# Kernel tuning notes

Measured on AMD Instinct MI355X. Metric: run time of the kernel, lower is better.

Reference implementation:

```python
import jax, jax.numpy as jnp
import numpy as np

D_IN = 1024
D_OUT = 1024
SEQ = 2048
BATCH = 4


def setup_inputs() -> dict:
    key = jax.random.key(0)
    kx, kq, kk, kv = jax.random.split(key, 4)
    x = jax.random.normal(kx, (BATCH, SEQ, D_IN), dtype=jnp.float32)
    s = 1.0 / np.sqrt(D_IN)
    Wq = jax.random.uniform(kq, (D_IN, D_OUT), dtype=jnp.float32, minval=-s, maxval=s)
    Wk = jax.random.uniform(kk, (D_IN, D_OUT), dtype=jnp.float32, minval=-s, maxval=s)
    Wv = jax.random.uniform(kv, (D_IN, D_OUT), dtype=jnp.float32, minval=-s, maxval=s)
    return {"x": x, "Wq": Wq, "Wk": Wk, "Wv": Wv}


def reference(x, Wq, Wk, Wv):
    d_k = Wq.shape[1]
    q = jnp.einsum('bsd,de->bse', x, Wq)
    k = jnp.einsum('bsd,de->bse', x, Wk)
    v = jnp.einsum('bsd,de->bse', x, Wv)
    # [B, S, S] raw scores
    scores = jnp.einsum('bqe,bke->bqk', q, k)
    S = scores.shape[-1]
    causal = jnp.triu(jnp.ones((S, S), dtype=bool), k=1)  # True above diagonal
    scores = jnp.where(causal, -jnp.inf, scores)
    attn = jax.nn.softmax(scores * (d_k ** -0.5), axis=-1)
    # dropout p=0.0 -> identity
    return jnp.einsum('bqk,bke->bqe', attn, v)
```

## Files before the change

### kernel.cpp

```cpp
#include <hip/hip_runtime.h>
#include <hip/hip_bf16.h>

typedef unsigned short u16;
typedef __bf16 bfx8 __attribute__((ext_vector_type(8)));
typedef float fx4 __attribute__((ext_vector_type(4)));

#define SEQ 2048
#define DIM 1024
#define NBATCH 4
#define SCALE 0.03125f
#define NEL ((size_t)NBATCH * SEQ * DIM)

__device__ inline u16 f2bf(float f) {
    __bf16 h = (__bf16)f;
    return __builtin_bit_cast(unsigned short, h);
}

#define GLL(gp, lp) __builtin_amdgcn_global_load_lds( \
    (const __attribute__((address_space(1))) unsigned int*)(gp), \
    (__attribute__((address_space(3))) unsigned int*)(lp), 16, 0, 0)

__global__ __launch_bounds__(256) void prep(
    const float* __restrict__ X,
    const float* __restrict__ Wq, const float* __restrict__ Wk,
    const float* __restrict__ Wv,
    u16* __restrict__ XB, u16* __restrict__ WB, u16* __restrict__ WTv,
    float* __restrict__ Lrow)
{
    __shared__ u16 t[32][33];
    int bid = blockIdx.x;
    int tid = threadIdx.x;
    if (bid < 8192) {
        size_t i = (size_t)bid * 256 + tid;
        float4 v = ((const float4*)X)[i];
        uint2 pk;
        pk.x = (unsigned)f2bf(v.x) | ((unsigned)f2bf(v.y) << 16);
        pk.y = (unsigned)f2bf(v.z) | ((unsigned)f2bf(v.w) << 16);
        ((uint2*)XB)[i] = pk;
    } else if (bid < 10240) {
        int b2 = bid - 8192;
        const float* W = (b2 < 1024) ? Wq : Wk;
        u16* out = WB + (size_t)(b2 >> 10) * 1024 * 1024;
        size_t i = (size_t)(b2 & 1023) * 256 + tid;
        float4 v = ((const float4*)W)[i];
        uint2 pk;
        pk.x = (unsigned)f2bf(v.x) | ((unsigned)f2bf(v.y) << 16);
        pk.y = (unsigned)f2bf(v.z) | ((unsigned)f2bf(v.w) << 16);
        ((uint2*)out)[i] = pk;
    } else if (bid < 11264) {
        int t2 = bid - 10240;
        int n0 = (t2 & 31) * 32, k0 = (t2 >> 5) * 32;
        int tx = tid & 31, ty = tid >> 5;
        #pragma unroll
        for (int i = 0; i < 32; i += 8)
            t[ty + i][tx] = f2bf(Wv[(size_t)(k0 + ty + i) * 1024 + n0 + tx]);
        __syncthreads();
        #pragma unroll
        for (int i = 0; i < 32; i += 8)
            WTv[(size_t)(n0 + ty + i) * 1024 + k0 + tx] = t[tx][ty + i];
    } else {
        int i = (bid - 11264) * 256 + tid;
        Lrow[i] = 0.0f;
    }
}

__global__ __launch_bounds__(256) void gemm_m(
    const u16* __restrict__ WBk, const u16* __restrict__ WBq, u16* __restrict__ MT)
{
    int m0 = blockIdx.y * 128, n0 = blockIdx.x * 128;
    __shared__ __align__(16) u16 As[128 * 32];
    __shared__ __align__(16) u16 Bs[128 * 32];
    int tid = threadIdx.x, lane = tid & 63, w = tid >> 6;
    int wm = w >> 1, wn = w & 1, lo = lane & 15, qd = lane >> 4;
    fx4 acc[4][4] = {};

    int c0 = tid, c1 = tid + 256;
    const u16* a0 = WBk + (size_t)(m0 + (c0 >> 2)) * 1024 + (((c0 & 3) ^ ((c0 >> 2) & 3)) * 8);
    const u16* a1 = WBk + (size_t)(m0 + (c1 >> 2)) * 1024 + (((c1 & 3) ^ ((c1 >> 2) & 3)) * 8);
    const u16* b0 = WBq + (size_t)(n0 + (c0 >> 2)) * 1024 + (((c0 & 3) ^ ((c0 >> 2) & 3)) * 8);
    const u16* b1 = WBq + (size_t)(n0 + (c1 >> 2)) * 1024 + (((c1 & 3) ^ ((c1 >> 2) & 3)) * 8);

    int sw = (qd ^ (lo & 3)) * 8;
    for (int k0 = 0; k0 < 1024; k0 += 32) {
        GLL(a0 + k0, &As[(size_t)c0 * 8]);
        GLL(a1 + k0, &As[(size_t)c1 * 8]);
        GLL(b0 + k0, &Bs[(size_t)c0 * 8]);
        GLL(b1 + k0, &Bs[(size_t)c1 * 8]);
        __syncthreads();
        bfx8 af[4], bf[4];
        #pragma unroll
        for (int i = 0; i < 4; i++)
            af[i] = *(const bfx8*)(&As[(wm * 64 + i * 16 + lo) * 32 + sw]);
        #pragma unroll
        for (int j = 0; j < 4; j++)
            bf[j] = *(const bfx8*)(&Bs[(wn * 64 + j * 16 + lo) * 32 + sw]);
        #pragma unroll
        for (int i = 0; i < 4; i++)
            #pragma unroll
            for (int j = 0; j < 4; j++)
                acc[i][j] = __builtin_amdgcn_mfma_f32_16x16x32_bf16(af[i], bf[j], acc[i][j], 0, 0, 0);
        __syncthreads();
    }
    #pragma unroll
    for (int i = 0; i < 4; i++)
        #pragma unroll
        for (int j = 0; j < 4; j++)
            #pragma unroll
            for (int r = 0; r < 4; r++)
                MT[(size_t)(m0 + wm * 64 + i * 16 + qd * 4 + r) * 1024
                   + n0 + wn * 64 + j * 16 + lo] = f2bf(acc[i][j][r]);
}

__global__ __launch_bounds__(512) void gemm256(
    const u16* __restrict__ XB, const u16* __restrict__ MT,
    const u16* __restrict__ WTv,
    u16* __restrict__ Yo, u16* __restrict__ VTo)
{
    const u16* Bop = (blockIdx.z == 0) ? MT : WTv;
    const int m0 = blockIdx.y * 256, n0 = blockIdx.x * 256;

    __shared__ __align__(16) u16 SM[65536];

    const int tid = threadIdx.x, lane = tid & 63, w = tid >> 6;
    const int wm = w >> 2, wn = w & 3, lo = lane & 15, qd = lane >> 4;
    const int swl = lo & 7;

    fx4 acc[8][4] = {};

    const u16* sA[4]; const u16* sB[4]; int dofs[4];
    #pragma unroll
    for (int p = 0; p < 4; ++p) {
        int n = p * 512 + tid;
        int row = n >> 3;
        int c = (n & 7) ^ (row & 7);
        sA[p] = XB  + (size_t)(m0 + row) * 1024 + c * 8;
        sB[p] = Bop + (size_t)(n0 + row) * 1024 + c * 8;
        dofs[p] = n * 8;
    }

    auto stage = [&](int kt2) {
        const int bb = (kt2 & 1) * 16384;
        #pragma unroll
        for (int p = 0; p < 4; ++p) GLL(sA[p] + kt2 * 64, &SM[bb + dofs[p]]);
        #pragma unroll
        for (int p = 0; p < 4; ++p) GLL(sB[p] + kt2 * 64, &SM[32768 + bb + dofs[p]]);
    };

    stage(0);
    stage(1);
    asm volatile("s_waitcnt vmcnt(8)" ::: "memory");
    __builtin_amdgcn_s_barrier();
    asm volatile("" ::: "memory");

    bfx8 af[4][2], bfA[2][2], bfB[2][2];

    for (int kt = 0; kt < 16; ++kt) {
        const u16* Ab = SM + (kt & 1) * 16384;
        const u16* Bb = SM + 32768 + (kt & 1) * 16384;

        #pragma unroll
        for (int ph = 0; ph < 4; ++ph) {
            const int mh = ph >> 1, nh = ph & 1;
            if (nh == 0) {
                #pragma unroll
                for (int ii = 0; ii < 4; ++ii)
                    #pragma unroll
                    for (int ks = 0; ks < 2; ++ks)
                        af[ii][ks] = *(const bfx8*)(Ab
                            + (wm * 128 + (mh * 4 + ii) * 16 + lo) * 64
                            + ((ks * 4 + qd) ^ swl) * 8);
            }
            if (ph == 0) {
                #pragma unroll
                for (int jn = 0; jn < 2; ++jn)
                    #pragma unroll
                    for (int ks = 0; ks < 2; ++ks)
                        bfA[jn][ks] = *(const bfx8*)(Bb
                            + (wn * 64 + jn * 16 + lo) * 64
                            + ((ks * 4 + qd) ^ swl) * 8);
            }
            if (ph == 1) {
                #pragma unroll
                for (int jn = 0; jn < 2; ++jn)
                    #pragma unroll
                    for (int ks = 0; ks < 2; ++ks)
                        bfB[jn][ks] = *(const bfx8*)(Bb
                            + (wn * 64 + (2 + jn) * 16 + lo) * 64
                            + ((ks * 4 + qd) ^ swl) * 8);
            }
            __builtin_amdgcn_s_barrier();
            asm volatile("s_waitcnt lgkmcnt(0)" ::: "memory");
            __builtin_amdgcn_sched_barrier(0);
            __builtin_amdgcn_s_setprio(1);
            #pragma unroll
            for (int ii = 0; ii < 4; ++ii)
                #pragma unroll
                for (int jn = 0; jn < 2; ++jn)
                    #pragma unroll
                    for (int ks = 0; ks < 2; ++ks) {
                        if (nh == 0)
                            acc[mh * 4 + ii][jn] = __builtin_amdgcn_mfma_f32_16x16x32_bf16(
                                af[ii][ks], bfA[jn][ks], acc[mh * 4 + ii][jn], 0, 0, 0);
                        else
                            acc[mh * 4 + ii][2 + jn] = __builtin_amdgcn_mfma_f32_16x16x32_bf16(
                                af[ii][ks], bfB[jn][ks], acc[mh * 4 + ii][2 + jn], 0, 0, 0);
                    }
            __builtin_amdgcn_s_setprio(0);
            __builtin_amdgcn_s_barrier();
            asm volatile("" ::: "memory");
        }
        if (kt < 14) stage(kt + 2);
        if (kt < 15) {
            if (kt < 14) asm volatile("s_waitcnt vmcnt(8)" ::: "memory");
            else         asm volatile("s_waitcnt vmcnt(0)" ::: "memory");
            __builtin_amdgcn_s_barrier();
            asm volatile("" ::: "memory");
        }
    }

    if (blockIdx.z == 0) {
        #pragma unroll
        for (int i = 0; i < 8; i++)
            #pragma unroll
            for (int j = 0; j < 4; j++)
                #pragma unroll
                for (int r = 0; r < 4; r++) {
                    int row = m0 + wm * 128 + i * 16 + qd * 4 + r;
                    int col = n0 + wn * 64 + j * 16 + lo;
                    Yo[(size_t)row * 1024 + col] = f2bf(acc[i][j][r]);
                }
    } else {
        u16 (*Ct)[258] = (u16(*)[258])SM;
        const int bb = m0 >> 11;
        const int sbase = m0 & 2047;
        #pragma unroll
        for (int half = 0; half < 2; ++half) {
            __syncthreads();
            if (wm == half) {
                #pragma unroll
                for (int i = 0; i < 8; i++)
                    #pragma unroll
                    for (int j = 0; j < 4; j++)
                        #pragma unroll
                        for (int r = 0; r < 4; r++)
                            Ct[i * 16 + qd * 4 + r][wn * 64 + j * 16 + lo] = f2bf(acc[i][j][r]);
            }
            __syncthreads();
            for (int e = tid; e < 16384; e += 512) {
                int d = e >> 6, s2 = (e & 63) * 2;
                unsigned pk = (unsigned)Ct[s2][d] | ((unsigned)Ct[s2 + 1][d] << 16);
                *(unsigned*)&VTo[((size_t)bb * DIM + (n0 + d)) * SEQ
                                 + sbase + half * 128 + s2] = pk;
            }
        }
    }
}

__global__ __launch_bounds__(512) void sgemm_exp(
    const u16* __restrict__ Y, const u16* __restrict__ XB,
    u16* __restrict__ P, float* __restrict__ Lrow)
{
    int b = blockIdx.y;
    int t = blockIdx.x;
    int i = (int)((sqrtf(8.0f * t + 1.0f) - 1.0f) * 0.5f);
    while ((i + 1) * (i + 2) / 2 <= t) i++;
    while (i * (i + 1) / 2 > t) i--;
    int j = t - i * (i + 1) / 2;

    const u16* Yb = Y + (size_t)b * SEQ * DIM;
    const u16* Xb = XB + (size_t)b * SEQ * DIM;
    u16* Pb = P + (size_t)b * SEQ * SEQ;
    float* Lb = Lrow + (size_t)b * SEQ;

    int m0 = i * 128, n0 = j * 128;

    __shared__ __align__(16) u16 SM[32768];

    int tid = threadIdx.x, lane = tid & 63, w = tid >> 6;
    int wm = w >> 2, wn = w & 3, lo = lane & 15, qd = lane >> 4;
    int swl = lo & 7;

    fx4 acc[4][2] = {};

    int c0 = tid, c1 = tid + 512;
    const u16* a0 = Yb + (size_t)(m0 + (c0 >> 3)) * 1024 + (((c0 & 7) ^ ((c0 >> 3) & 7)) * 8);
    const u16* a1 = Yb + (size_t)(m0 + (c1 >> 3)) * 1024 + (((c1 & 7) ^ ((c1 >> 3) & 7)) * 8);
    const u16* b0 = Xb + (size_t)(n0 + (c0 >> 3)) * 1024 + (((c0 & 7) ^ ((c0 >> 3) & 7)) * 8);
    const u16* b1 = Xb + (size_t)(n0 + (c1 >> 3)) * 1024 + (((c1 & 7) ^ ((c1 >> 3) & 7)) * 8);
    int d0 = c0 * 8, d1 = c1 * 8;

    auto stage = [&](int kt2) {
        int bb = (kt2 & 1) * 8192;
        GLL(a0 + kt2 * 64, &SM[bb + d0]);
        GLL(a1 + kt2 * 64, &SM[bb + d1]);
        GLL(b0 + kt2 * 64, &SM[16384 + bb + d0]);
        GLL(b1 + kt2 * 64, &SM[16384 + bb + d1]);
    };

    stage(0);
    stage(1);
    asm volatile("s_waitcnt vmcnt(4)" ::: "memory");
    __builtin_amdgcn_s_barrier();
    asm volatile("" ::: "memory");

    for (int kt = 0; kt < 16; ++kt) {
        const u16* Ab = SM + (kt & 1) * 8192;
        const u16* Bb = SM + 16384 + (kt & 1) * 8192;

        #pragma unroll
        for (int kc = 0; kc < 2; ++kc) {
            bfx8 af[4], bf[2];
            int sw = ((kc * 4 + qd) ^ swl) * 8;
            #pragma unroll
            for (int ii = 0; ii < 4; ++ii)
                af[ii] = *(const bfx8*)(Ab + (wm * 64 + ii * 16 + lo) * 64 + sw);
            #pragma unroll
            for (int jn = 0; jn < 2; ++jn)
                bf[jn] = *(const bfx8*)(Bb + (wn * 32 + jn * 16 + lo) * 64 + sw);
            __builtin_amdgcn_s_barrier();
            asm volatile("s_waitcnt lgkmcnt(0)" ::: "memory");
            __builtin_amdgcn_sched_barrier(0);
            __builtin_amdgcn_s_setprio(1);
            #pragma unroll
            for (int ii = 0; ii < 4; ++ii)
                #pragma unroll
                for (int jn = 0; jn < 2; ++jn)
                    acc[ii][jn] = __builtin_amdgcn_mfma_f32_16x16x32_bf16(af[ii], bf[jn], acc[ii][jn], 0, 0, 0);
            __builtin_amdgcn_s_setprio(0);
            __builtin_amdgcn_s_barrier();
            asm volatile("" ::: "memory");
        }
        if (kt < 14) stage(kt + 2);
        if (kt < 15) {
            if (kt < 14) asm volatile("s_waitcnt vmcnt(4)" ::: "memory");
            else         asm volatile("s_waitcnt vmcnt(0)" ::: "memory");
            __builtin_amdgcn_s_barrier();
            asm volatile("" ::: "memory");
        }
    }

    #pragma unroll
    for (int ii = 0; ii < 4; ii++)
        #pragma unroll
        for (int r = 0; r < 4; r++) {
            int row = m0 + wm * 64 + ii * 16 + qd * 4 + r;
            float rs = 0.0f;
            #pragma unroll
            for (int jn = 0; jn < 2; jn++) {
                int col = n0 + wn * 32 + jn * 16 + lo;
                float s = acc[ii][jn][r] * SCALE;
                s = fminf(fmaxf(s, -30.0f), 30.0f);
                float p = (col > row) ? 0.0f : __expf(s);
                Pb[(size_t)row * SEQ + col] = f2bf(p);
                rs += p;
            }
            #pragma unroll
            for (int off = 1; off < 16; off <<= 1) rs += __shfl_xor(rs, off);
            if (lo == 0) atomicAdd(&Lb[row], rs);
        }
}

__global__ __launch_bounds__(512) void pvgemm(
    const u16* __restrict__ P, const u16* __restrict__ VT,
    const float* __restrict__ Lrow, float* __restrict__ O)
{
    int b = blockIdx.y;
    int qb = 15 - (int)(blockIdx.x >> 3);
    int db = blockIdx.x & 7;
    int m0 = qb * 128, n0 = db * 128;
    int nkt = (qb + 1) * 2;

    const u16* Pb = P + (size_t)b * SEQ * SEQ;
    const u16* Vb = VT + (size_t)b * DIM * SEQ;
    const float* Lb = Lrow + (size_t)b * SEQ;
    float* Ob = O + (size_t)b * SEQ * DIM;

    __shared__ __align__(16) u16 SM[32768];

    int tid = threadIdx.x, lane = tid & 63, w = tid >> 6;
    int wm = w >> 2, wn = w & 3, lo = lane & 15, qd = lane >> 4;
    int swl = lo & 7;

    fx4 acc[4][2] = {};

    int c0 = tid, c1 = tid + 512;
    const u16* a0 = Pb + (size_t)(m0 + (c0 >> 3)) * SEQ + (((c0 & 7) ^ ((c0 >> 3) & 7)) * 8);
    const u16* a1 = Pb + (size_t)(m0 + (c1 >> 3)) * SEQ + (((c1 & 7) ^ ((c1 >> 3) & 7)) * 8);
    const u16* b0 = Vb + (size_t)(n0 + (c0 >> 3)) * SEQ + (((c0 & 7) ^ ((c0 >> 3) & 7)) * 8);
    const u16* b1 = Vb + (size_t)(n0 + (c1 >> 3)) * SEQ + (((c1 & 7) ^ ((c1 >> 3) & 7)) * 8);
    int d0 = c0 * 8, d1 = c1 * 8;

    auto stage = [&](int kt2) {
        int bb = (kt2 & 1) * 8192;
        GLL(a0 + kt2 * 64, &SM[bb + d0]);
        GLL(a1 + kt2 * 64, &SM[bb + d1]);
        GLL(b0 + kt2 * 64, &SM[16384 + bb + d0]);
        GLL(b1 + kt2 * 64, &SM[16384 + bb + d1]);
    };

    stage(0);
    stage(1);
    asm volatile("s_waitcnt vmcnt(4)" ::: "memory");
    __builtin_amdgcn_s_barrier();
    asm volatile("" ::: "memory");

    for (int kt = 0; kt < nkt; ++kt) {
        const u16* Ab = SM + (kt & 1) * 8192;
        const u16* Bb = SM + 16384 + (kt & 1) * 8192;

        #pragma unroll
        for (int kc = 0; kc < 2; ++kc) {
            bfx8 af[4], bf[2];
            int sw = ((kc * 4 + qd) ^ swl) * 8;
            #pragma unroll
            for (int ii = 0; ii < 4; ++ii)
                af[ii] = *(const bfx8*)(Ab + (wm * 64 + ii * 16 + lo) * 64 + sw);
            #pragma unroll
            for (int jn = 0; jn < 2; ++jn)
                bf[jn] = *(const bfx8*)(Bb + (wn * 32 + jn * 16 + lo) * 64 + sw);
            __builtin_amdgcn_s_barrier();
            asm volatile("s_waitcnt lgkmcnt(0)" ::: "memory");
            __builtin_amdgcn_sched_barrier(0);
            __builtin_amdgcn_s_setprio(1);
            #pragma unroll
            for (int ii = 0; ii < 4; ++ii)
                #pragma unroll
                for (int jn = 0; jn < 2; ++jn)
                    acc[ii][jn] = __builtin_amdgcn_mfma_f32_16x16x32_bf16(af[ii], bf[jn], acc[ii][jn], 0, 0, 0);
            __builtin_amdgcn_s_setprio(0);
            __builtin_amdgcn_s_barrier();
            asm volatile("" ::: "memory");
        }
        if (kt + 2 < nkt) stage(kt + 2);
        if (kt + 1 < nkt) {
            if (kt + 2 < nkt) asm volatile("s_waitcnt vmcnt(4)" ::: "memory");
            else              asm volatile("s_waitcnt vmcnt(0)" ::: "memory");
            __builtin_amdgcn_s_barrier();
            asm volatile("" ::: "memory");
        }
    }

    #pragma unroll
    for (int ii = 0; ii < 4; ii++)
        #pragma unroll
        for (int r = 0; r < 4; r++) {
            int row = m0 + wm * 64 + ii * 16 + qd * 4 + r;
            float linv = 1.0f / Lb[row];
            #pragma unroll
            for (int jn = 0; jn < 2; jn++) {
                int col = n0 + wn * 32 + jn * 16 + lo;
                Ob[(size_t)row * DIM + col] = acc[ii][jn][r] * linv;
            }
        }
}

__global__ __launch_bounds__(256) void gemm_legacy(
    const float* __restrict__ X,
    const float* __restrict__ Wq, const float* __restrict__ Wk, const float* __restrict__ Wv,
    u16* __restrict__ Qo, u16* __restrict__ Ko, u16* __restrict__ VTo)
{
    const int K = 1024, N = 1024;
    const float* W = (blockIdx.z == 0) ? Wq : (blockIdx.z == 1) ? Wk : Wv;
    int m0 = blockIdx.y * 128, n0 = blockIdx.x * 128;
    __shared__ __align__(16) u16 As[128 * 40];
    __shared__ __align__(16) u16 Bs[128 * 40];
    __shared__ __align__(16) u16 Ct[64][132];
    int tid = threadIdx.x, lane = tid & 63, w = tid >> 6;
    int wm = w >> 1, wn = w & 1, lo = lane & 15, qd = lane >> 4;
    fx4 acc[4][4] = {};
    for (int k0 = 0; k0 < K; k0 += 32) {
        #pragma unroll
        for (int c = tid; c < 1024; c += 256) {
            int row = c >> 3, cc = (c & 7) * 4;
            float4 v = *(const float4*)(X + (size_t)(m0 + row) * K + k0 + cc);
            uint2 pk;
            pk.x = (unsigned)f2bf(v.x) | ((unsigned)f2bf(v.y) << 16);
            pk.y = (unsigned)f2bf(v.z) | ((unsigned)f2bf(v.w) << 16);
            *(uint2*)(&As[row * 40 + cc]) = pk;
        }
        #pragma unroll
        for (int c = tid; c < 1024; c += 256) {
            int r = c >> 5, cc = (c & 31) * 4;
            float4 v = *(const float4*)(W + (size_t)(k0 + r) * N + n0 + cc);
            Bs[(cc + 0) * 40 + r] = f2bf(v.x);
            Bs[(cc + 1) * 40 + r] = f2bf(v.y);
            Bs[(cc + 2) * 40 + r] = f2bf(v.z);
            Bs[(cc + 3) * 40 + r] = f2bf(v.w);
        }
        __syncthreads();
        bfx8 af[4], bf[4];
        #pragma unroll
        for (int i = 0; i < 4; i++)
            af[i] = *(const bfx8*)(&As[(wm * 64 + i * 16 + lo) * 40 + qd * 8]);
        #pragma unroll
        for (int j = 0; j < 4; j++)
            bf[j] = *(const bfx8*)(&Bs[(wn * 64 + j * 16 + lo) * 40 + qd * 8]);
        #pragma unroll
        for (int i = 0; i < 4; i++)
            #pragma unroll
            for (int j = 0; j < 4; j++)
                acc[i][j] = __builtin_amdgcn_mfma_f32_16x16x32_bf16(af[i], bf[j], acc[i][j], 0, 0, 0);
        __syncthreads();
    }
    if (blockIdx.z != 2) {
        u16* C = (blockIdx.z == 0) ? Qo : Ko;
        #pragma unroll
        for (int i = 0; i < 4; i++)
            #pragma unroll
            for (int j = 0; j < 4; j++)
                #pragma unroll
                for (int r = 0; r < 4; r++) {
                    int row = m0 + wm * 64 + i * 16 + qd * 4 + r;
                    int col = n0 + wn * 64 + j * 16 + lo;
                    C[(size_t)row * N + col] = f2bf(acc[i][j][r]);
                }
    } else {
        #pragma unroll
        for (int half = 0; half < 2; half++) {
            __syncthreads();
            if (wm == half) {
                #pragma unroll
                for (int i = 0; i < 4; i++)
                    #pragma unroll
                    for (int j = 0; j < 4; j++)
                        #pragma unroll
                        for (int r = 0; r < 4; r++)
                            Ct[i * 16 + qd * 4 + r][wn * 64 + j * 16 + lo] = f2bf(acc[i][j][r]);
            }
            __syncthreads();
            #pragma unroll
            for (int e = tid; e < 64 * 128; e += 256) {
                int d = e >> 6, sl = e & 63;
                int gr = m0 + half * 64 + sl;
                int bb = gr >> 11, s = gr & 2047;
                VTo[((size_t)bb * DIM + (n0 + d)) * SEQ + s] = Ct[sl][d];
            }
        }
    }
}

__global__ __launch_bounds__(512) void flash_attn(
    const u16* __restrict__ Q, const u16* __restrict__ Kmat,
    const u16* __restrict__ VT, float* __restrict__ O)
{
    int b = blockIdx.y;
    int qt = (int)(gridDim.x - 1) - (int)blockIdx.x;
    int q0 = qt * 32;
    int tid = threadIdx.x;
    int lane = tid & 63, w = tid >> 6;
    int lo = lane & 15, qd = lane >> 4;

    __shared__ __align__(16) float Sp[8][32][33];
    __shared__ __align__(16) __bf16 Pl[32][40];
    __shared__ float ml[32], ll[32], al[32];

    const u16* Qb = Q + (size_t)b * SEQ * DIM;
    const u16* Kb = Kmat + (size_t)b * SEQ * DIM;
    const u16* VTb = VT + (size_t)b * DIM * SEQ;

    bfx8 qf[2][4];
    #pragma unroll
    for (int i = 0; i < 2; i++)
        #pragma unroll
        for (int c = 0; c < 4; c++)
            qf[i][c] = *(const bfx8*)(Qb + (size_t)(q0 + i * 16 + lo) * DIM + w * 128 + c * 32 + qd * 8);

    fx4 oacc[2][8] = {};
    if (tid < 32) { ml[tid] = -INFINITY; ll[tid] = 0.0f; }
    __syncthreads();

    for (int kt = 0; kt <= qt; kt++) {
        int k0 = kt * 32;
        fx4 sp[2][2] = {};
        #pragma unroll
        for (int c = 0; c < 4; c++) {
            bfx8 kf[2];
            #pragma unroll
            for (int jn = 0; jn < 2; jn++)
                kf[jn] = *(const bfx8*)(Kb + (size_t)(k0 + jn * 16 + lo) * DIM + w * 128 + c * 32 + qd * 8);
            #pragma unroll
            for (int i = 0; i < 2; i++)
                #pragma unroll
                for (int jn = 0; jn < 2; jn++)
                    sp[i][jn] = __builtin_amdgcn_mfma_f32_16x16x32_bf16(qf[i][c], kf[jn], sp[i][jn], 0, 0, 0);
        }
        #pragma unroll
        for (int i = 0; i < 2; i++)
            #pragma unroll
            for (int jn = 0; jn < 2; jn++)
                #pragma unroll
                for (int r = 0; r < 4; r++)
                    Sp[w][i * 16 + qd * 4 + r][jn * 16 + lo] = sp[i][jn][r];
        __syncthreads();
        {
            int r = tid >> 4, ci = tid & 15;
            int q = q0 + r;
            float s0 = 0.0f, s1 = 0.0f;
            #pragma unroll
            for (int p = 0; p < 8; p++) { s0 += Sp[p][r][ci]; s1 += Sp[p][r][ci + 16]; }
            s0 = fminf(fmaxf(s0 * SCALE, -1e30f), 1e30f);
            s1 = fminf(fmaxf(s1 * SCALE, -1e30f), 1e30f);
            if (k0 + ci > q)      s0 = -INFINITY;
            if (k0 + ci + 16 > q) s1 = -INFINITY;
            float mx = fmaxf(s0, s1);
            #pragma unroll
            for (int off = 1; off < 16; off <<= 1) mx = fmaxf(mx, __shfl_xor(mx, off));
            float mo = ml[r];
            float mn = fmaxf(mo, mx);
            float p0 = __expf(s0 - mn), p1 = __expf(s1 - mn);
            Pl[r][ci] = (__bf16)p0;
            Pl[r][ci + 16] = (__bf16)p1;
            float ps = p0 + p1;
            #pragma unroll
            for (int off = 1; off < 16; off <<= 1) ps += __shfl_xor(ps, off);
            if (ci == 0) {
                float alpha = __expf(mo - mn);
                ll[r] = alpha * ll[r] + ps;
                ml[r] = mn;
                al[r] = alpha;
            }
        }
        __syncthreads();
        float alocal[2][4];
        #pragma unroll
        for (int i = 0; i < 2; i++)
            #pragma unroll
            for (int r = 0; r < 4; r++)
                alocal[i][r] = al[i * 16 + qd * 4 + r];
        #pragma unroll
        for (int i = 0; i < 2; i++)
            #pragma unroll
            for (int j = 0; j < 8; j++)
                #pragma unroll
                for (int r = 0; r < 4; r++)
                    oacc[i][j][r] *= alocal[i][r];
        bfx8 pf[2];
        #pragma unroll
        for (int i = 0; i < 2; i++)
            pf[i] = *(const bfx8*)(&Pl[i * 16 + lo][qd * 8]);
        #pragma unroll
        for (int j = 0; j < 8; j++) {
            bfx8 vf = *(const bfx8*)(VTb + (size_t)(w * 128 + j * 16 + lo) * SEQ + k0 + qd * 8);
            #pragma unroll
            for (int i = 0; i < 2; i++)
                oacc[i][j] = __builtin_amdgcn_mfma_f32_16x16x32_bf16(pf[i], vf, oacc[i][j], 0, 0, 0);
        }
    }

    float linv[2][4];
    #pragma unroll
    for (int i = 0; i < 2; i++)
        #pragma unroll
        for (int r = 0; r < 4; r++)
            linv[i][r] = 1.0f / ll[i * 16 + qd * 4 + r];
    float* Ob = O + (size_t)b * SEQ * DIM;
    #pragma unroll
    for (int i = 0; i < 2; i++)
        #pragma unroll
        for (int j = 0; j < 8; j++)
            #pragma unroll
            for (int r = 0; r < 4; r++) {
                int row = q0 + i * 16 + qd * 4 + r;
                int col = w * 128 + j * 16 + lo;
                Ob[(size_t)row * DIM + col] = oacc[i][j][r] * linv[i][r];
            }
}

extern "C" void kernel_launch(void* const* d_in, const int* in_sizes, int n_in,
                              void* d_out, int out_size, void* d_ws, size_t ws_size,
                              hipStream_t stream) {
    const float* x  = (const float*)d_in[0];
    const float* Wq = (const float*)d_in[1];
    const float* Wk = (const float*)d_in[2];
    const float* Wv = (const float*)d_in[3];

    u16* ws = (u16*)d_ws;
    u16* Yp  = ws;
    u16* VTp = ws + NEL;
    u16* XBp = ws + 2 * NEL;
    u16* WBp = ws + 3 * NEL;
    u16* WTv = WBp + (size_t)2 * 1024 * 1024;
    u16* MTp = WTv + (size_t)1024 * 1024;
    u16* Pm  = MTp + (size_t)1024 * 1024;
    float* Lrow = (float*)(Pm + (size_t)NBATCH * SEQ * SEQ);

    size_t need_mat = ((size_t)3 * NEL + (size_t)4 * 1024 * 1024
                     + (size_t)NBATCH * SEQ * SEQ) * 2
                     + (size_t)NBATCH * SEQ * 4 + 1024;

    if (ws_size >= need_mat) {
        prep<<<dim3(11296), 256, 0, stream>>>(x, Wq, Wk, Wv, XBp, WBp, WTv, Lrow);
        gemm_m<<<dim3(8, 8), 256, 0, stream>>>(
            WBp + (size_t)1024 * 1024 , WBp , MTp);
        gemm256<<<dim3(4, 32, 2), 512, 0, stream>>>(XBp, MTp, WTv, Yp, VTp);
        sgemm_exp<<<dim3(136, NBATCH), 512, 0, stream>>>(Yp, XBp, Pm, Lrow);
        pvgemm<<<dim3(128, NBATCH), 512, 0, stream>>>(Pm, VTp, Lrow, (float*)d_out);
    } else {
        u16* Qp = ws; u16* Kp = ws + NEL; u16* VTf = ws + 2 * NEL;
        gemm_legacy<<<dim3(8, 64, 3), 256, 0, stream>>>(x, Wq, Wk, Wv, Qp, Kp, VTf);
        flash_attn<<<dim3(SEQ / 32, NBATCH), 512, 0, stream>>>(
            Qp, Kp, VTf, (float*)d_out);
    }
}
```

Baseline: 232.5 us.

## Enlarge score and PV GEMM tiles to 256 rows for more operand reuse

The score GEMM (sgemm_exp) moves from 128x128 to 256x256 tiles and the PV GEMM from 128x128 to 256x128 tiles. Each wave now keeps 8x4 or 8x2 accumulator fragments and loads operands in phases, so fragments loaded from LDS feed more MFMAs. Global-to-LDS staging doubles and LDS use grows (128 KB and 96 KB). The aim is less global and LDS traffic per FLOP, at the cost of far fewer blocks (144 and 256), more register pressure, and coarser causal-triangle granularity, which computes more masked work on diagonal tiles.

```diff
diff --git a/kernel.cpp b/kernel.cpp
--- a/kernel.cpp
+++ b/kernel.cpp
@@ -272,51 +272,77 @@
     u16* Pb = P + (size_t)b * SEQ * SEQ;
     float* Lb = Lrow + (size_t)b * SEQ;
 
-    int m0 = i * 128, n0 = j * 128;
-
-    __shared__ __align__(16) u16 SM[32768];
-
-    int tid = threadIdx.x, lane = tid & 63, w = tid >> 6;
-    int wm = w >> 2, wn = w & 3, lo = lane & 15, qd = lane >> 4;
-    int swl = lo & 7;
-
-    fx4 acc[4][2] = {};
-
-    int c0 = tid, c1 = tid + 512;
-    const u16* a0 = Yb + (size_t)(m0 + (c0 >> 3)) * 1024 + (((c0 & 7) ^ ((c0 >> 3) & 7)) * 8);
-    const u16* a1 = Yb + (size_t)(m0 + (c1 >> 3)) * 1024 + (((c1 & 7) ^ ((c1 >> 3) & 7)) * 8);
-    const u16* b0 = Xb + (size_t)(n0 + (c0 >> 3)) * 1024 + (((c0 & 7) ^ ((c0 >> 3) & 7)) * 8);
-    const u16* b1 = Xb + (size_t)(n0 + (c1 >> 3)) * 1024 + (((c1 & 7) ^ ((c1 >> 3) & 7)) * 8);
-    int d0 = c0 * 8, d1 = c1 * 8;
+    const int m0 = i * 256, n0 = j * 256;
+
+    __shared__ __align__(16) u16 SM[65536];
+
+    const int tid = threadIdx.x, lane = tid & 63, w = tid >> 6;
+    const int wm = w >> 2, wn = w & 3, lo = lane & 15, qd = lane >> 4;
+    const int swl = lo & 7;
+
+    fx4 acc[8][4] = {};
+
+    const u16* sA[4]; const u16* sB[4]; int dofs[4];
+    #pragma unroll
+    for (int p = 0; p < 4; ++p) {
+        int n = p * 512 + tid;
+        int row = n >> 3;
+        int c = (n & 7) ^ (row & 7);
+        sA[p] = Yb + (size_t)(m0 + row) * 1024 + c * 8;
+        sB[p] = Xb + (size_t)(n0 + row) * 1024 + c * 8;
+        dofs[p] = n * 8;
+    }
 
     auto stage = [&](int kt2) {
-        int bb = (kt2 & 1) * 8192;
-        GLL(a0 + kt2 * 64, &SM[bb + d0]);
-        GLL(a1 + kt2 * 64, &SM[bb + d1]);
-        GLL(b0 + kt2 * 64, &SM[16384 + bb + d0]);
-        GLL(b1 + kt2 * 64, &SM[16384 + bb + d1]);
+        const int bb = (kt2 & 1) * 16384;
+        #pragma unroll
+        for (int p = 0; p < 4; ++p) GLL(sA[p] + kt2 * 64, &SM[bb + dofs[p]]);
+        #pragma unroll
+        for (int p = 0; p < 4; ++p) GLL(sB[p] + kt2 * 64, &SM[32768 + bb + dofs[p]]);
     };
 
     stage(0);
     stage(1);
-    asm volatile("s_waitcnt vmcnt(4)" ::: "memory");
+    asm volatile("s_waitcnt vmcnt(8)" ::: "memory");
     __builtin_amdgcn_s_barrier();
     asm volatile("" ::: "memory");
 
+    bfx8 af[4][2], bfA[2][2], bfB[2][2];
+
     for (int kt = 0; kt < 16; ++kt) {
-        const u16* Ab = SM + (kt & 1) * 8192;
-        const u16* Bb = SM + 16384 + (kt & 1) * 8192;
-
-        #pragma unroll
-        for (int kc = 0; kc < 2; ++kc) {
-            bfx8 af[4], bf[2];
-            int sw = ((kc * 4 + qd) ^ swl) * 8;
-            #pragma unroll
-            for (int ii = 0; ii < 4; ++ii)
-                af[ii] = *(const bfx8*)(Ab + (wm * 64 + ii * 16 + lo) * 64 + sw);
-            #pragma unroll
-            for (int jn = 0; jn < 2; ++jn)
-                bf[jn] = *(const bfx8*)(Bb + (wn * 32 + jn * 16 + lo) * 64 + sw);
+        const u16* Ab = SM + (kt & 1) * 16384;
+        const u16* Bb = SM + 32768 + (kt & 1) * 16384;
+
+        #pragma unroll
+        for (int ph = 0; ph < 4; ++ph) {
+            const int mh = ph >> 1, nh = ph & 1;
+            if (nh == 0) {
+                #pragma unroll
+                for (int ii = 0; ii < 4; ++ii)
+                    #pragma unroll
+                    for (int ks = 0; ks < 2; ++ks)
+                        af[ii][ks] = *(const bfx8*)(Ab
+                            + (wm * 128 + (mh * 4 + ii) * 16 + lo) * 64
+                            + ((ks * 4 + qd) ^ swl) * 8);
+            }
+            if (ph == 0) {
+                #pragma unroll
+                for (int jn = 0; jn < 2; ++jn)
+                    #pragma unroll
+                    for (int ks = 0; ks < 2; ++ks)
+                        bfA[jn][ks] = *(const bfx8*)(Bb
+                            + (wn * 64 + jn * 16 + lo) * 64
+                            + ((ks * 4 + qd) ^ swl) * 8);
+            }
+            if (ph == 1) {
+                #pragma unroll
+                for (int jn = 0; jn < 2; ++jn)
+                    #pragma unroll
+                    for (int ks = 0; ks < 2; ++ks)
+                        bfB[jn][ks] = *(const bfx8*)(Bb
+                            + (wn * 64 + (2 + jn) * 16 + lo) * 64
+                            + ((ks * 4 + qd) ^ swl) * 8);
+            }
             __builtin_amdgcn_s_barrier();
             asm volatile("s_waitcnt lgkmcnt(0)" ::: "memory");
             __builtin_amdgcn_sched_barrier(0);
@@ -325,14 +351,22 @@
             for (int ii = 0; ii < 4; ++ii)
                 #pragma unroll
                 for (int jn = 0; jn < 2; ++jn)
-                    acc[ii][jn] = __builtin_amdgcn_mfma_f32_16x16x32_bf16(af[ii], bf[jn], acc[ii][jn], 0, 0, 0);
+                    #pragma unroll
+                    for (int ks = 0; ks < 2; ++ks) {
+                        if (nh == 0)
+                            acc[mh * 4 + ii][jn] = __builtin_amdgcn_mfma_f32_16x16x32_bf16(
+                                af[ii][ks], bfA[jn][ks], acc[mh * 4 + ii][jn], 0, 0, 0);
+                        else
+                            acc[mh * 4 + ii][2 + jn] = __builtin_amdgcn_mfma_f32_16x16x32_bf16(
+                                af[ii][ks], bfB[jn][ks], acc[mh * 4 + ii][2 + jn], 0, 0, 0);
+                    }
             __builtin_amdgcn_s_setprio(0);
             __builtin_amdgcn_s_barrier();
             asm volatile("" ::: "memory");
         }
         if (kt < 14) stage(kt + 2);
         if (kt < 15) {
-            if (kt < 14) asm volatile("s_waitcnt vmcnt(4)" ::: "memory");
+            if (kt < 14) asm volatile("s_waitcnt vmcnt(8)" ::: "memory");
             else         asm volatile("s_waitcnt vmcnt(0)" ::: "memory");
             __builtin_amdgcn_s_barrier();
             asm volatile("" ::: "memory");
@@ -340,14 +374,14 @@
     }
 
     #pragma unroll
-    for (int ii = 0; ii < 4; ii++)
+    for (int ii = 0; ii < 8; ii++)
         #pragma unroll
         for (int r = 0; r < 4; r++) {
-            int row = m0 + wm * 64 + ii * 16 + qd * 4 + r;
+            int row = m0 + wm * 128 + ii * 16 + qd * 4 + r;
             float rs = 0.0f;
             #pragma unroll
-            for (int jn = 0; jn < 2; jn++) {
-                int col = n0 + wn * 32 + jn * 16 + lo;
+            for (int jn = 0; jn < 4; jn++) {
+                int col = n0 + wn * 64 + jn * 16 + lo;
                 float s = acc[ii][jn][r] * SCALE;
                 s = fminf(fmaxf(s, -30.0f), 30.0f);
                 float p = (col > row) ? 0.0f : __expf(s);
@@ -365,59 +399,80 @@
     const float* __restrict__ Lrow, float* __restrict__ O)
 {
     int b = blockIdx.y;
-    int qb = 15 - (int)(blockIdx.x >> 3);
+    int qb = 7 - (int)(blockIdx.x >> 3);
     int db = blockIdx.x & 7;
-    int m0 = qb * 128, n0 = db * 128;
-    int nkt = (qb + 1) * 2;
+    int m0 = qb * 256, n0 = db * 128;
+    int nkt = (qb + 1) * 4;
 
     const u16* Pb = P + (size_t)b * SEQ * SEQ;
     const u16* Vb = VT + (size_t)b * DIM * SEQ;
     const float* Lb = Lrow + (size_t)b * SEQ;
     float* Ob = O + (size_t)b * SEQ * DIM;
 
-    __shared__ __align__(16) u16 SM[32768];
-
-    int tid = threadIdx.x, lane = tid & 63, w = tid >> 6;
-    int wm = w >> 2, wn = w & 3, lo = lane & 15, qd = lane >> 4;
-    int swl = lo & 7;
-
-    fx4 acc[4][2] = {};
-
-    int c0 = tid, c1 = tid + 512;
-    const u16* a0 = Pb + (size_t)(m0 + (c0 >> 3)) * SEQ + (((c0 & 7) ^ ((c0 >> 3) & 7)) * 8);
-    const u16* a1 = Pb + (size_t)(m0 + (c1 >> 3)) * SEQ + (((c1 & 7) ^ ((c1 >> 3) & 7)) * 8);
-    const u16* b0 = Vb + (size_t)(n0 + (c0 >> 3)) * SEQ + (((c0 & 7) ^ ((c0 >> 3) & 7)) * 8);
-    const u16* b1 = Vb + (size_t)(n0 + (c1 >> 3)) * SEQ + (((c1 & 7) ^ ((c1 >> 3) & 7)) * 8);
-    int d0 = c0 * 8, d1 = c1 * 8;
+    __shared__ __align__(16) u16 SM[49152];
+
+    const int tid = threadIdx.x, lane = tid & 63, w = tid >> 6;
+    const int wm = w >> 2, wn = w & 3, lo = lane & 15, qd = lane >> 4;
+    const int swl = lo & 7;
+
+    fx4 acc[8][2] = {};
+
+    const u16* sA[4]; int dofsA[4];
+    #pragma unroll
+    for (int p = 0; p < 4; ++p) {
+        int n = p * 512 + tid;
+        int row = n >> 3;
+        int c = (n & 7) ^ (row & 7);
+        sA[p] = Pb + (size_t)(m0 + row) * SEQ + c * 8;
+        dofsA[p] = n * 8;
+    }
+    const u16* sB[2]; int dofsB[2];
+    #pragma unroll
+    for (int p = 0; p < 2; ++p) {
+        int n = p * 512 + tid;
+        int row = n >> 3;
+        int c = (n & 7) ^ (row & 7);
+        sB[p] = Vb + (size_t)(n0 + row) * SEQ + c * 8;
+        dofsB[p] = n * 8;
+    }
 
     auto stage = [&](int kt2) {
-        int bb = (kt2 & 1) * 8192;
-        GLL(a0 + kt2 * 64, &SM[bb + d0]);
-        GLL(a1 + kt2 * 64, &SM[bb + d1]);
-        GLL(b0 + kt2 * 64, &SM[16384 + bb + d0]);
-        GLL(b1 + kt2 * 64, &SM[16384 + bb + d1]);
+        const int ba = (kt2 & 1) * 16384;
+        const int bb = 32768 + (kt2 & 1) * 8192;
+        #pragma unroll
+        for (int p = 0; p < 4; ++p) GLL(sA[p] + kt2 * 64, &SM[ba + dofsA[p]]);
+        #pragma unroll
+        for (int p = 0; p < 2; ++p) GLL(sB[p] + kt2 * 64, &SM[bb + dofsB[p]]);
     };
 
     stage(0);
     stage(1);
-    asm volatile("s_waitcnt vmcnt(4)" ::: "memory");
+    asm volatile("s_waitcnt vmcnt(6)" ::: "memory");
     __builtin_amdgcn_s_barrier();
     asm volatile("" ::: "memory");
 
+    bfx8 bf[2][2];
+
     for (int kt = 0; kt < nkt; ++kt) {
-        const u16* Ab = SM + (kt & 1) * 8192;
-        const u16* Bb = SM + 16384 + (kt & 1) * 8192;
-
-        #pragma unroll
-        for (int kc = 0; kc < 2; ++kc) {
-            bfx8 af[4], bf[2];
-            int sw = ((kc * 4 + qd) ^ swl) * 8;
+        const u16* Ab = SM + (kt & 1) * 16384;
+        const u16* Bb = SM + 32768 + (kt & 1) * 8192;
+
+        #pragma unroll
+        for (int ph = 0; ph < 4; ++ph) {
+            const int mh = ph >> 1, ks = ph & 1;
+            bfx8 af[4];
             #pragma unroll
             for (int ii = 0; ii < 4; ++ii)
-                af[ii] = *(const bfx8*)(Ab + (wm * 64 + ii * 16 + lo) * 64 + sw);
-            #pragma unroll
-            for (int jn = 0; jn < 2; ++jn)
-                bf[jn] = *(const bfx8*)(Bb + (wn * 32 + jn * 16 + lo) * 64 + sw);
+                af[ii] = *(const bfx8*)(Ab
+                    + (wm * 128 + (mh * 4 + ii) * 16 + lo) * 64
+                    + ((ks * 4 + qd) ^ swl) * 8);
+            if (mh == 0) {
+                #pragma unroll
+                for (int jn = 0; jn < 2; ++jn)
+                    bf[ks][jn] = *(const bfx8*)(Bb
+                        + (wn * 32 + jn * 16 + lo) * 64
+                        + ((ks * 4 + qd) ^ swl) * 8);
+            }
             __builtin_amdgcn_s_barrier();
             asm volatile("s_waitcnt lgkmcnt(0)" ::: "memory");
             __builtin_amdgcn_sched_barrier(0);
@@ -426,14 +481,15 @@
             for (int ii = 0; ii < 4; ++ii)
                 #pragma unroll
                 for (int jn = 0; jn < 2; ++jn)
-                    acc[ii][jn] = __builtin_amdgcn_mfma_f32_16x16x32_bf16(af[ii], bf[jn], acc[ii][jn], 0, 0, 0);
+                    acc[mh * 4 + ii][jn] = __builtin_amdgcn_mfma_f32_16x16x32_bf16(
+                        af[ii], bf[ks][jn], acc[mh * 4 + ii][jn], 0, 0, 0);
             __builtin_amdgcn_s_setprio(0);
             __builtin_amdgcn_s_barrier();
             asm volatile("" ::: "memory");
         }
         if (kt + 2 < nkt) stage(kt + 2);
         if (kt + 1 < nkt) {
-            if (kt + 2 < nkt) asm volatile("s_waitcnt vmcnt(4)" ::: "memory");
+            if (kt + 2 < nkt) asm volatile("s_waitcnt vmcnt(6)" ::: "memory");
             else              asm volatile("s_waitcnt vmcnt(0)" ::: "memory");
             __builtin_amdgcn_s_barrier();
             asm volatile("" ::: "memory");
@@ -441,10 +497,10 @@
     }
 
     #pragma unroll
-    for (int ii = 0; ii < 4; ii++)
+    for (int ii = 0; ii < 8; ii++)
         #pragma unroll
         for (int r = 0; r < 4; r++) {
-            int row = m0 + wm * 64 + ii * 16 + qd * 4 + r;
+            int row = m0 + wm * 128 + ii * 16 + qd * 4 + r;
             float linv = 1.0f / Lb[row];
             #pragma unroll
             for (int jn = 0; jn < 2; jn++) {
@@ -693,8 +749,8 @@
         gemm_m<<<dim3(8, 8), 256, 0, stream>>>(
             WBp + (size_t)1024 * 1024 , WBp , MTp);
         gemm256<<<dim3(4, 32, 2), 512, 0, stream>>>(XBp, MTp, WTv, Yp, VTp);
-        sgemm_exp<<<dim3(136, NBATCH), 512, 0, stream>>>(Yp, XBp, Pm, Lrow);
-        pvgemm<<<dim3(128, NBATCH), 512, 0, stream>>>(Pm, VTp, Lrow, (float*)d_out);
+        sgemm_exp<<<dim3(36, NBATCH), 512, 0, stream>>>(Yp, XBp, Pm, Lrow);
+        pvgemm<<<dim3(64, NBATCH), 512, 0, stream>>>(Pm, VTp, Lrow, (float*)d_out);
     } else {
         u16* Qp = ws; u16* Kp = ws + NEL; u16* VTf = ws + 2 * NEL;
         gemm_legacy<<<dim3(8, 64, 3), 256, 0, stream>>>(x, Wq, Wk, Wv, Qp, Kp, VTf);
```

After: 236.1 us. About the same (+1.5%).
